# Kernel tuning notes

Measured on AMD Instinct MI355X. Metric: run time of the kernel, lower is better.

Reference implementation:

```python
import jax, jax.numpy as jnp
import numpy as np

N_HEADS, N_LEVELS, N_POINTS = 8, 3, 4


def _bilinear_sample(valf, Hl, Wl, grid):
    """torch.F.grid_sample(mode='bilinear', padding_mode='zeros', align_corners=False).
    valf: [B, nH, hd, Hl*Wl] flattened per-head value map
    grid: [B, Q, nH, P, 2] normalized (x, y) in [-1, 1]
    returns [B, nH, hd, Q, P]
    """
    B, Q, nH, P, _ = grid.shape
    hd = valf.shape[2]
    # unnormalize (align_corners=False)
    ix = ((grid[..., 0] + 1.0) * Wl - 1.0) * 0.5  # [B,Q,nH,P]
    iy = ((grid[..., 1] + 1.0) * Hl - 1.0) * 0.5
    x0 = jnp.floor(ix); y0 = jnp.floor(iy)
    x1 = x0 + 1.0;      y1 = y0 + 1.0
    # corner weights
    w00 = (x1 - ix) * (y1 - iy)
    w01 = (ix - x0) * (y1 - iy)
    w10 = (x1 - ix) * (iy - y0)
    w11 = (ix - x0) * (iy - y0)

    def gather(xi, yi):
        inb = (xi >= 0) & (xi <= Wl - 1) & (yi >= 0) & (yi <= Hl - 1)  # zero padding
        xc = jnp.clip(xi, 0, Wl - 1).astype(jnp.int32)
        yc = jnp.clip(yi, 0, Hl - 1).astype(jnp.int32)
        idx = yc * Wl + xc                              # [B,Q,nH,P]
        idx = idx.transpose(0, 2, 1, 3).reshape(B, nH, 1, Q * P)
        idx = jnp.broadcast_to(idx, (B, nH, hd, Q * P))
        g = jnp.take_along_axis(valf, idx, axis=3)      # [B,nH,hd,Q*P]
        g = g.reshape(B, nH, hd, Q, P)
        mask = inb.transpose(0, 2, 1, 3)[:, :, None, :, :]
        return g * mask

    def w_(w):  # [B,Q,nH,P] -> [B,nH,1,Q,P]
        return w.transpose(0, 2, 1, 3)[:, :, None, :, :]

    return (gather(x0, y0) * w_(w00) + gather(x1, y0) * w_(w01)
            + gather(x0, y1) * w_(w10) + gather(x1, y1) * w_(w11))


def _deform_attn(query, feats, reference_points,
                 W_off, b_off, W_attn, b_attn, W_val, b_val, W_out, b_out):
    B, Q, D = query.shape
    nH, L, P = N_HEADS, N_LEVELS, N_POINTS
    hd = D // nH
    # sampling offsets: tanh * 0.5
    off = jnp.tanh(query @ W_off + b_off).reshape(B, Q, nH, L, P, 2) * 0.5
    # attention weights: softmax over levels*points
    aw = jax.nn.softmax((query @ W_attn + b_attn).reshape(B, Q, nH, L * P), axis=-1)
    aw = aw.reshape(B, Q, nH, L, P)

    out = jnp.zeros((B, Q, nH, hd), dtype=query.dtype)
    for lvl, feat in enumerate(feats):
        Hl, Wl = feat.shape[2], feat.shape[3]
        # value projection on flattened map
        v = feat.reshape(B, D, Hl * Wl).transpose(0, 2, 1) @ W_val + b_val  # [B,S,D]
        valf = v.reshape(B, Hl * Wl, nH, hd).transpose(0, 2, 3, 1)          # [B,nH,hd,S]
        grid = (reference_points[:, :, None, None, :] + off[:, :, :, lvl]) * 2.0 - 1.0  # [B,Q,nH,P,2]
        sampled = _bilinear_sample(valf, Hl, Wl, grid)                      # [B,nH,hd,Q,P]
        w = aw[:, :, :, lvl].transpose(0, 2, 1, 3)[:, :, None, :, :]        # [B,nH,1,Q,P]
        out = out + (sampled * w).sum(-1).transpose(0, 3, 1, 2)             # [B,Q,nH,hd]
    return out.reshape(B, Q, D) @ W_out + b_out


def setup_inputs() -> dict:
    key = jax.random.key(0)
    ks = jax.random.split(key, 13)
    B, Q, D = 4, 8400, 256
    return {
        "query": jax.random.normal(ks[0], (B, Q, D), jnp.float32),
        "feat0": jax.random.normal(ks[1], (B, D, 80, 80), jnp.float32),
        "feat1": jax.random.normal(ks[2], (B, D, 40, 40), jnp.float32),
        "feat2": jax.random.normal(ks[3], (B, D, 20, 20), jnp.float32),
        "reference_points": jax.random.uniform(ks[4], (B, Q, 2), jnp.float32),
        "W_off": jax.random.normal(ks[5], (D, N_HEADS * N_LEVELS * N_POINTS * 2), jnp.float32) * 0.02,
        "b_off": jax.random.normal(ks[6], (N_HEADS * N_LEVELS * N_POINTS * 2,), jnp.float32) * 0.02,
        "W_attn": jax.random.normal(ks[7], (D, N_HEADS * N_LEVELS * N_POINTS), jnp.float32) * 0.02,
        "b_attn": jax.random.normal(ks[8], (N_HEADS * N_LEVELS * N_POINTS,), jnp.float32) * 0.02,
        "W_val": jax.random.normal(ks[9], (D, D), jnp.float32) * (1.0 / np.sqrt(D)),
        "b_val": jnp.zeros((D,), jnp.float32),
        "W_out": jax.random.normal(ks[10], (D, D), jnp.float32) * (1.0 / np.sqrt(D)),
        "b_out": jnp.zeros((D,), jnp.float32),
    }


def reference(query, feat0, feat1, feat2, reference_points,
              W_off, b_off, W_attn, b_attn, W_val, b_val, W_out, b_out):
    return _deform_attn(query, [feat0, feat1, feat2], reference_points,
                        W_off, b_off, W_attn, b_attn, W_val, b_val, W_out, b_out)
```

## Files before the change

### kernel.cpp

```cpp
#include <hip/hip_runtime.h>
#include <math.h>

#define NH    8
#define NPT   4
#define DIM   256
#define NQ    8400
#define BATCH 4
#define STOT  8400
#define MQ    (BATCH * NQ)

typedef __attribute__((ext_vector_type(8))) short  s16x8;
typedef __attribute__((ext_vector_type(8))) unsigned short u16x8;
typedef __attribute__((ext_vector_type(4))) float  f32x4;

static __device__ __forceinline__ unsigned short f2bf(float x) {
    union { float f; unsigned u; } v; v.f = x;
    unsigned r = v.u + 0x7fffu + ((v.u >> 16) & 1u);
    return (unsigned short)(r >> 16);
}
static __device__ __forceinline__ float bf2f(unsigned short h) {
    union { float f; unsigned u; } v; v.u = ((unsigned)h) << 16;
    return v.f;
}

__global__ __launch_bounds__(256) void tp_w(
    const float* __restrict__ W, int Nw,
    unsigned short* __restrict__ outH, unsigned short* __restrict__ outL, int n0)
{
    __shared__ float tile[32][33];
    const int t = threadIdx.x;
    const int nb = blockIdx.x * 32, k0 = blockIdx.y * 32;
    const int c = t & 31, r = t >> 5;
    #pragma unroll
    for (int i = 0; i < 4; ++i) {
        int k = k0 + r + i * 8, n = nb + c;
        tile[r + i * 8][c] = (n < Nw) ? W[(size_t)k * Nw + n] : 0.f;
    }
    __syncthreads();
    #pragma unroll
    for (int i = 0; i < 4; ++i) {
        int n = nb + r + i * 8, k = k0 + c;
        if (n < Nw) {
            float x = tile[c][r + i * 8];
            unsigned short h = f2bf(x);
            outH[(size_t)(n0 + n) * 256 + k] = h;
            if (outL) outL[(size_t)(n0 + n) * 256 + k] = f2bf(x - bf2f(h));
        }
    }
}

__global__ __launch_bounds__(256) void tp_feat(
    const float* __restrict__ feat, int S, int base,
    unsigned short* __restrict__ Abf)
{
    __shared__ float tile[32][33];
    const int t = threadIdx.x;
    const int s0 = blockIdx.x * 32, k0 = blockIdx.y * 32, b = blockIdx.z;
    const int c = t & 31, r = t >> 5;
    #pragma unroll
    for (int i = 0; i < 4; ++i) {
        int k = k0 + r + i * 8, s = s0 + c;
        tile[r + i * 8][c] = (s < S) ? feat[((size_t)b * 256 + k) * S + s] : 0.f;
    }
    __syncthreads();
    #pragma unroll
    for (int i = 0; i < 4; ++i) {
        int s = s0 + r + i * 8, k = k0 + c;
        if (s < S)
            Abf[((size_t)(b * STOT + base + s)) * 256 + k] = f2bf(tile[c][r + i * 8]);
    }
}

__global__ void cat_bias(const float* __restrict__ boff, const float* __restrict__ battn,
                         float* __restrict__ bcat)
{
    int t = blockIdx.x * 256 + threadIdx.x;
    if (t < 192) bcat[t] = boff[t];
    else if (t < 288) bcat[t] = battn[t - 192];
}

template<bool SPLIT, int MODE>
__global__ __launch_bounds__(256) void gemm_bt(
    const void* __restrict__ Aptr,
    const unsigned short* __restrict__ Bh, const unsigned short* __restrict__ Bl,
    const float* __restrict__ bias, void* __restrict__ Cptr,
    int M, int N, int K)
{
    __shared__ unsigned short Ah[128 * 40];
    __shared__ unsigned short Bs[128 * 40];
    __shared__ unsigned short Al[SPLIT ? 128 * 40 : 8];
    __shared__ unsigned short Blo[SPLIT ? 128 * 40 : 8];

    const int t = threadIdx.x;
    const int bn = blockIdx.x * 128, bm = blockIdx.y * 128;
    const int lane = t & 63, w = t >> 6;
    const int wm = (w & 1) * 64, wn = (w >> 1) * 64;
    const int l15 = lane & 15, quad = lane >> 4;

    f32x4 acc[4][4];
    #pragma unroll
    for (int i = 0; i < 4; ++i)
        #pragma unroll
        for (int j = 0; j < 4; ++j)
            acc[i][j] = (f32x4){0.f, 0.f, 0.f, 0.f};

    for (int k0 = 0; k0 < K; k0 += 32) {
        #pragma unroll
        for (int cc = 0; cc < 2; ++cc) {
            int cid = t + cc * 256;
            int r = cid >> 2, s = cid & 3;
            int gr = bm + r; if (gr > M - 1) gr = M - 1;
            if constexpr (SPLIT) {
                const float* ap = (const float*)Aptr + (size_t)gr * K + k0 + s * 8;
                float4 f0 = *(const float4*)ap;
                float4 f1 = *(const float4*)(ap + 4);
                float xs[8] = {f0.x, f0.y, f0.z, f0.w, f1.x, f1.y, f1.z, f1.w};
                u16x8 hv, lv;
                #pragma unroll
                for (int e = 0; e < 8; ++e) {
                    unsigned short h = f2bf(xs[e]);
                    hv[e] = h;
                    lv[e] = f2bf(xs[e] - bf2f(h));
                }
                *(u16x8*)&Ah[r * 40 + s * 8] = hv;
                *(u16x8*)&Al[r * 40 + s * 8] = lv;
            } else {
                u16x8 v = *(const u16x8*)((const unsigned short*)Aptr + (size_t)gr * K + k0 + s * 8);
                *(u16x8*)&Ah[r * 40 + s * 8] = v;
            }
        }
        #pragma unroll
        for (int cc = 0; cc < 2; ++cc) {
            int cid = t + cc * 256;
            int r = cid >> 2, s = cid & 3;
            int gn = bn + r; if (gn > N - 1) gn = N - 1;
            u16x8 v = *(const u16x8*)&Bh[(size_t)gn * K + k0 + s * 8];
            *(u16x8*)&Bs[r * 40 + s * 8] = v;
            if constexpr (SPLIT) {
                u16x8 vl = *(const u16x8*)&Bl[(size_t)gn * K + k0 + s * 8];
                *(u16x8*)&Blo[r * 40 + s * 8] = vl;
            }
        }
        __syncthreads();

        s16x8 af[4], bf[4];
        #pragma unroll
        for (int mt = 0; mt < 4; ++mt)
            af[mt] = *(const s16x8*)&Ah[(wm + mt * 16 + l15) * 40 + quad * 8];
        #pragma unroll
        for (int nt = 0; nt < 4; ++nt)
            bf[nt] = *(const s16x8*)&Bs[(wn + nt * 16 + l15) * 40 + quad * 8];

        if constexpr (SPLIT) {
            s16x8 alf[4], blf[4];
            #pragma unroll
            for (int mt = 0; mt < 4; ++mt)
                alf[mt] = *(const s16x8*)&Al[(wm + mt * 16 + l15) * 40 + quad * 8];
            #pragma unroll
            for (int nt = 0; nt < 4; ++nt)
                blf[nt] = *(const s16x8*)&Blo[(wn + nt * 16 + l15) * 40 + quad * 8];
            #pragma unroll
            for (int mt = 0; mt < 4; ++mt)
                #pragma unroll
                for (int nt = 0; nt < 4; ++nt) {
                    acc[mt][nt] = __builtin_amdgcn_mfma_f32_16x16x32_bf16(af[mt], bf[nt], acc[mt][nt], 0, 0, 0);
                    acc[mt][nt] = __builtin_amdgcn_mfma_f32_16x16x32_bf16(af[mt], blf[nt], acc[mt][nt], 0, 0, 0);
                    acc[mt][nt] = __builtin_amdgcn_mfma_f32_16x16x32_bf16(alf[mt], bf[nt], acc[mt][nt], 0, 0, 0);
                }
        } else {
            #pragma unroll
            for (int mt = 0; mt < 4; ++mt)
                #pragma unroll
                for (int nt = 0; nt < 4; ++nt)
                    acc[mt][nt] = __builtin_amdgcn_mfma_f32_16x16x32_bf16(af[mt], bf[nt], acc[mt][nt], 0, 0, 0);
        }
        __syncthreads();
    }

    #pragma unroll
    for (int nt = 0; nt < 4; ++nt) {
        int col = bn + wn + nt * 16 + l15;
        float bv = (col < N) ? bias[col] : 0.f;
        #pragma unroll
        for (int mt = 0; mt < 4; ++mt) {
            int row0 = bm + wm + mt * 16 + quad * 4;
            #pragma unroll
            for (int r = 0; r < 4; ++r) {
                int row = row0 + r;
                if (row < M && col < N) {
                    float v = acc[mt][nt][r] + bv;
                    if constexpr (MODE == 0) {
                        ((float*)Cptr)[(size_t)row * N + col] = v;
                    } else {
                        int bb = row / STOT, s = row - bb * STOT;
                        int h = col >> 5, c = col & 31;
                        ((unsigned short*)Cptr)[(((size_t)(bb * 8 + h)) * STOT + s) * 32 + c] = f2bf(v);
                    }
                }
            }
        }
    }
}

__global__ __launch_bounds__(256) void sample_v3(
    const unsigned short* __restrict__ valb,
    const float* __restrict__ raw,
    const float* __restrict__ refp,
    unsigned short* __restrict__ out_bf)
{
    const int bq0 = blockIdx.x * 8;
    const int b = bq0 / NQ;
    const int t = threadIdx.x;

    __shared__ int   s_idx[8][96][4];
    __shared__ float s_w[8][96][4];
    __shared__ float s_m[8][8];
    __shared__ float s_inv[8][8];

    if (t < 64) {
        int q = t >> 3, h = t & 7;
        const float* a = &raw[(size_t)(bq0 + q) * 288 + 192 + h * 12];
        float m = a[0];
        #pragma unroll
        for (int j = 1; j < 12; ++j) m = fmaxf(m, a[j]);
        float s = 0.f;
        #pragma unroll
        for (int j = 0; j < 12; ++j) s += expf(a[j] - m);
        s_m[q][h] = m;
        s_inv[q][h] = 1.f / s;
    }
    __syncthreads();

    for (int i = t; i < 768; i += 256) {
        int q = i / 96, p = i - q * 96;
        int h = p / 12, lp = p - h * 12, l = lp >> 2;
        const int dims[3]   = {80, 40, 20};
        const int bases_[3] = {0, 6400, 8000};
        int Wl = dims[l], base = bases_[l];
        size_t ro = (size_t)(bq0 + q) * 288;
        float logit = raw[ro + 192 + p];
        float aw = expf(logit - s_m[q][h]) * s_inv[q][h];
        float rawx = raw[ro + h * 24 + lp * 2 + 0];
        float rawy = raw[ro + h * 24 + lp * 2 + 1];
        float rx = refp[(size_t)(bq0 + q) * 2];
        float ry = refp[(size_t)(bq0 + q) * 2 + 1];
        float ix = (rx + tanhf(rawx) * 0.5f) * Wl - 0.5f;
        float iy = (ry + tanhf(rawy) * 0.5f) * Wl - 0.5f;
        float x0f = floorf(ix), y0f = floorf(iy);
        float fx = ix - x0f, fy = iy - y0f;
        int x0 = (int)x0f, y0 = (int)y0f;
        float w00 = (1.f - fx) * (1.f - fy) * aw;
        float w01 = fx * (1.f - fy) * aw;
        float w10 = (1.f - fx) * fy * aw;
        float w11 = fx * fy * aw;
        bool vx0 = (unsigned)x0 < (unsigned)Wl;
        bool vx1 = (unsigned)(x0 + 1) < (unsigned)Wl;
        bool vy0 = (unsigned)y0 < (unsigned)Wl;
        bool vy1 = (unsigned)(y0 + 1) < (unsigned)Wl;
        int row0 = base + y0 * Wl, row1 = row0 + Wl;
        s_idx[q][p][0] = (vx0 && vy0) ? row0 + x0     : 0;  s_w[q][p][0] = (vx0 && vy0) ? w00 : 0.f;
        s_idx[q][p][1] = (vx1 && vy0) ? row0 + x0 + 1 : 0;  s_w[q][p][1] = (vx1 && vy0) ? w01 : 0.f;
        s_idx[q][p][2] = (vx0 && vy1) ? row1 + x0     : 0;  s_w[q][p][2] = (vx0 && vy1) ? w10 : 0.f;
        s_idx[q][p][3] = (vx1 && vy1) ? row1 + x0 + 1 : 0;  s_w[q][p][3] = (vx1 && vy1) ? w11 : 0.f;
    }
    __syncthreads();

    const int q = t >> 5;
    const int h = (t >> 2) & 7;
    const int l4 = t & 3;
    const unsigned short* vb = valb + ((size_t)(b * 8 + h) * STOT) * 32 + l4 * 8;
    const int*   ip = &s_idx[q][h * 12][0];
    const float* wp = &s_w[q][h * 12][0];
    float acc[8] = {};
    #pragma unroll
    for (int pp = 0; pp < 4; ++pp) {
        int   ix[12]; float ww[12]; u16x8 v[12];
        #pragma unroll
        for (int k = 0; k < 12; ++k) { ix[k] = ip[pp * 12 + k]; ww[k] = wp[pp * 12 + k]; }
        #pragma unroll
        for (int k = 0; k < 12; ++k) v[k] = *(const u16x8*)(vb + (size_t)ix[k] * 32);
        #pragma unroll
        for (int k = 0; k < 12; ++k)
            #pragma unroll
            for (int c = 0; c < 8; ++c)
                acc[c] = fmaf(ww[k], bf2f(v[k][c]), acc[c]);
    }

    u16x8 ob;
    #pragma unroll
    for (int c = 0; c < 8; ++c) ob[c] = f2bf(acc[c]);
    *(u16x8*)&out_bf[(size_t)(bq0 + q) * 256 + h * 32 + l4 * 8] = ob;
}

extern "C" void kernel_launch(void* const* d_in, const int* in_sizes, int n_in,
                              void* d_out, int out_size, void* d_ws, size_t ws_size,
                              hipStream_t stream)
{
    const float* query  = (const float*)d_in[0];
    const float* feat0  = (const float*)d_in[1];
    const float* feat1  = (const float*)d_in[2];
    const float* feat2  = (const float*)d_in[3];
    const float* refp   = (const float*)d_in[4];
    const float* W_off  = (const float*)d_in[5];
    const float* b_off  = (const float*)d_in[6];
    const float* W_attn = (const float*)d_in[7];
    const float* b_attn = (const float*)d_in[8];
    const float* W_val  = (const float*)d_in[9];
    const float* b_val  = (const float*)d_in[10];
    const float* W_out  = (const float*)d_in[11];
    const float* b_out  = (const float*)d_in[12];
    float* out = (float*)d_out;

    unsigned short* valb = (unsigned short*)d_ws;
    float*          raw  = (float*)(valb + (size_t)MQ * 256);
    unsigned short* Abf  = (unsigned short*)(raw + (size_t)MQ * 288);
    unsigned short* outb = Abf;
    unsigned short* Wvt  = Abf + (size_t)MQ * 256;
    unsigned short* Wot  = Wvt + 256 * 256;
    unsigned short* Wch  = Wot + 256 * 256;
    unsigned short* Wcl  = Wch + 288 * 256;
    float*          bcat = (float*)(Wcl + 288 * 256);

    dim3 blk(256);

    tp_w<<<dim3(8, 8), blk, 0, stream>>>(W_val, 256, Wvt, nullptr, 0);
    tp_w<<<dim3(8, 8), blk, 0, stream>>>(W_out, 256, Wot, nullptr, 0);
    tp_w<<<dim3(6, 8), blk, 0, stream>>>(W_off, 192, Wch, Wcl, 0);
    tp_w<<<dim3(3, 8), blk, 0, stream>>>(W_attn, 96, Wch, Wcl, 192);
    cat_bias<<<dim3(2), blk, 0, stream>>>(b_off, b_attn, bcat);
    tp_feat<<<dim3(200, 8, BATCH), blk, 0, stream>>>(feat0, 6400, 0, Abf);
    tp_feat<<<dim3(50, 8, BATCH), blk, 0, stream>>>(feat1, 1600, 6400, Abf);
    tp_feat<<<dim3(13, 8, BATCH), blk, 0, stream>>>(feat2, 400, 8000, Abf);

    gemm_bt<false, 1><<<dim3(2, 263), blk, 0, stream>>>(Abf, Wvt, nullptr, b_val, valb, MQ, 256, 256);
    gemm_bt<true, 0><<<dim3(3, 263), blk, 0, stream>>>(query, Wch, Wcl, bcat, raw, MQ, 288, 256);
    sample_v3<<<dim3(MQ / 8), blk, 0, stream>>>(valb, raw, refp, outb);
    gemm_bt<false, 0><<<dim3(2, 263), blk, 0, stream>>>(outb, Wot, nullptr, b_out, out, MQ, 256, 256);
}
```

Baseline: 281.0 us.

## Merge prep and projection kernels into fewer launches, store attention logits in bf16

Collapses the four weight-transpose launches and the bias concat into one prep kernel. The three feature transposes and the query hi/lo bf16 split now run in one kernel. The value and offset/attention projection GEMMs become a single launch, and the sampler uses an XCD-aware block-to-query mapping and reads attention logits stored as bf16. This cuts launch count and tail effects, at the cost of extra memory traffic for the pre-split query buffers and reduced logit precision.

```diff
diff --git a/kernel.cpp b/kernel.cpp
--- a/kernel.cpp
+++ b/kernel.cpp
@@ -2,7 +2,6 @@
 #include <math.h>
 
 #define NH    8
-#define NPT   4
 #define DIM   256
 #define NQ    8400
 #define BATCH 4
@@ -23,13 +22,32 @@
     return v.f;
 }
 
-__global__ __launch_bounds__(256) void tp_w(
-    const float* __restrict__ W, int Nw,
-    unsigned short* __restrict__ outH, unsigned short* __restrict__ outL, int n0)
-{
+__global__ __launch_bounds__(256) void prep_w(
+    const float* __restrict__ W_val, const float* __restrict__ W_out,
+    const float* __restrict__ W_off, const float* __restrict__ W_attn,
+    const float* __restrict__ b_off, const float* __restrict__ b_attn,
+    unsigned short* __restrict__ Wvt, unsigned short* __restrict__ Wot,
+    unsigned short* __restrict__ Wch, unsigned short* __restrict__ Wcl,
+    float* __restrict__ bcat)
+{
+    const int z = blockIdx.z;
+    const int t = threadIdx.x;
+    if (z == 4) {
+        if (blockIdx.x == 0 && blockIdx.y == 0)
+            for (int i = t; i < 288; i += 256)
+                bcat[i] = (i < 192) ? b_off[i] : b_attn[i - 192];
+        return;
+    }
+    const float* W; unsigned short *oH, *oL; int Nw, n0;
+    switch (z) {
+        case 0:  W = W_val;  oH = Wvt; oL = nullptr; Nw = 256; n0 = 0;   break;
+        case 1:  W = W_out;  oH = Wot; oL = nullptr; Nw = 256; n0 = 0;   break;
+        case 2:  W = W_off;  oH = Wch; oL = Wcl;     Nw = 192; n0 = 0;   break;
+        default: W = W_attn; oH = Wch; oL = Wcl;     Nw = 96;  n0 = 192; break;
+    }
+    const int nb = blockIdx.x * 32, k0 = blockIdx.y * 32;
+    if (nb >= Nw) return;
     __shared__ float tile[32][33];
-    const int t = threadIdx.x;
-    const int nb = blockIdx.x * 32, k0 = blockIdx.y * 32;
     const int c = t & 31, r = t >> 5;
     #pragma unroll
     for (int i = 0; i < 4; ++i) {
@@ -43,54 +61,189 @@
         if (n < Nw) {
             float x = tile[c][r + i * 8];
             unsigned short h = f2bf(x);
-            outH[(size_t)(n0 + n) * 256 + k] = h;
-            if (outL) outL[(size_t)(n0 + n) * 256 + k] = f2bf(x - bf2f(h));
-        }
-    }
-}
-
-__global__ __launch_bounds__(256) void tp_feat(
-    const float* __restrict__ feat, int S, int base,
-    unsigned short* __restrict__ Abf)
-{
+            oH[(size_t)(n0 + n) * 256 + k] = h;
+            if (oL) oL[(size_t)(n0 + n) * 256 + k] = f2bf(x - bf2f(h));
+        }
+    }
+}
+
+__global__ __launch_bounds__(256) void prep_af(
+    const float* __restrict__ feat0, const float* __restrict__ feat1,
+    const float* __restrict__ feat2, const float* __restrict__ query,
+    unsigned short* __restrict__ Abf,
+    unsigned short* __restrict__ Qh, unsigned short* __restrict__ Ql)
+{
+    const int z = blockIdx.z;
+    const int t = threadIdx.x;
+    if (z >= 4) {
+        int lid = (z - 4) * 263 * 8 + blockIdx.x * 8 + blockIdx.y;
+        size_t idx = (size_t)lid * 1024 + t * 4;
+        if (idx < (size_t)MQ * 256) {
+            float4 q = *(const float4*)(query + idx);
+            float xs[4] = {q.x, q.y, q.z, q.w};
+            ushort4 hv, lv;
+            unsigned short h;
+            h = f2bf(xs[0]); hv.x = h; lv.x = f2bf(xs[0] - bf2f(h));
+            h = f2bf(xs[1]); hv.y = h; lv.y = f2bf(xs[1] - bf2f(h));
+            h = f2bf(xs[2]); hv.z = h; lv.z = f2bf(xs[2] - bf2f(h));
+            h = f2bf(xs[3]); hv.w = h; lv.w = f2bf(xs[3] - bf2f(h));
+            *(ushort4*)(Qh + idx) = hv;
+            *(ushort4*)(Ql + idx) = lv;
+        }
+        return;
+    }
+    const int b = z;
+    const int s0 = blockIdx.x * 32, k0 = blockIdx.y * 32;
+    const float* f0b = feat0 + (size_t)b * 256 * 6400;
+    const float* f1b = feat1 + (size_t)b * 256 * 1600;
+    const float* f2b = feat2 + (size_t)b * 256 * 400;
     __shared__ float tile[32][33];
-    const int t = threadIdx.x;
-    const int s0 = blockIdx.x * 32, k0 = blockIdx.y * 32, b = blockIdx.z;
     const int c = t & 31, r = t >> 5;
     #pragma unroll
     for (int i = 0; i < 4; ++i) {
-        int k = k0 + r + i * 8, s = s0 + c;
-        tile[r + i * 8][c] = (s < S) ? feat[((size_t)b * 256 + k) * S + s] : 0.f;
+        int rr = r + i * 8;
+        int s = s0 + c;
+        float v = 0.f;
+        if (s < 8400) {
+            const float* fp; int S, sl;
+            if (s < 6400)      { fp = f0b; S = 6400; sl = s; }
+            else if (s < 8000) { fp = f1b; S = 1600; sl = s - 6400; }
+            else               { fp = f2b; S = 400;  sl = s - 8000; }
+            v = fp[(size_t)(k0 + rr) * S + sl];
+        }
+        tile[rr][c] = v;
     }
     __syncthreads();
     #pragma unroll
     for (int i = 0; i < 4; ++i) {
         int s = s0 + r + i * 8, k = k0 + c;
-        if (s < S)
-            Abf[((size_t)(b * STOT + base + s)) * 256 + k] = f2bf(tile[c][r + i * 8]);
-    }
-}
-
-__global__ void cat_bias(const float* __restrict__ boff, const float* __restrict__ battn,
-                         float* __restrict__ bcat)
-{
-    int t = blockIdx.x * 256 + threadIdx.x;
-    if (t < 192) bcat[t] = boff[t];
-    else if (t < 288) bcat[t] = battn[t - 192];
-}
-
-template<bool SPLIT, int MODE>
-__global__ __launch_bounds__(256) void gemm_bt(
-    const void* __restrict__ Aptr,
-    const unsigned short* __restrict__ Bh, const unsigned short* __restrict__ Bl,
-    const float* __restrict__ bias, void* __restrict__ Cptr,
-    int M, int N, int K)
+        if (s < 8400)
+            Abf[((size_t)b * 8400 + s) * 256 + k] = f2bf(tile[c][r + i * 8]);
+    }
+}
+
+__global__ __launch_bounds__(256) void gemm_vr(
+    const unsigned short* __restrict__ Abf,
+    const unsigned short* __restrict__ Qh, const unsigned short* __restrict__ Ql,
+    const unsigned short* __restrict__ Wvt,
+    const unsigned short* __restrict__ Wch, const unsigned short* __restrict__ Wcl,
+    const float* __restrict__ b_val, const float* __restrict__ bcat,
+    unsigned short* __restrict__ valb, float* __restrict__ raw_off,
+    unsigned short* __restrict__ attnb)
 {
     __shared__ unsigned short Ah[128 * 40];
     __shared__ unsigned short Bs[128 * 40];
-    __shared__ unsigned short Al[SPLIT ? 128 * 40 : 8];
-    __shared__ unsigned short Blo[SPLIT ? 128 * 40 : 8];
-
+    __shared__ unsigned short Al[128 * 40];
+    __shared__ unsigned short Bl2[128 * 40];
+
+    const bool split = blockIdx.x >= 2;
+    const int bn = split ? (blockIdx.x - 2) * 128 : blockIdx.x * 128;
+    const int bm = blockIdx.y * 128;
+    const int N = split ? 288 : 256;
+    const unsigned short* Ag = split ? Qh : Abf;
+    const unsigned short* Bg = split ? Wch : Wvt;
+
+    const int t = threadIdx.x;
+    const int lane = t & 63, w = t >> 6;
+    const int wm = (w & 1) * 64, wn = (w >> 1) * 64;
+    const int l15 = lane & 15, quad = lane >> 4;
+
+    f32x4 acc[4][4];
+    #pragma unroll
+    for (int i = 0; i < 4; ++i)
+        #pragma unroll
+        for (int j = 0; j < 4; ++j)
+            acc[i][j] = (f32x4){0.f, 0.f, 0.f, 0.f};
+
+    for (int k0 = 0; k0 < 256; k0 += 32) {
+        #pragma unroll
+        for (int cc = 0; cc < 2; ++cc) {
+            int cid = t + cc * 256;
+            int r = cid >> 2, s = cid & 3;
+            int gr = bm + r; if (gr > MQ - 1) gr = MQ - 1;
+            u16x8 v = *(const u16x8*)(Ag + (size_t)gr * 256 + k0 + s * 8);
+            *(u16x8*)&Ah[r * 40 + s * 8] = v;
+            if (split) {
+                u16x8 vl = *(const u16x8*)(Ql + (size_t)gr * 256 + k0 + s * 8);
+                *(u16x8*)&Al[r * 40 + s * 8] = vl;
+            }
+            int gn = bn + r; if (gn > N - 1) gn = N - 1;
+            u16x8 bv = *(const u16x8*)(Bg + (size_t)gn * 256 + k0 + s * 8);
+            *(u16x8*)&Bs[r * 40 + s * 8] = bv;
+            if (split) {
+                u16x8 bl = *(const u16x8*)(Wcl + (size_t)gn * 256 + k0 + s * 8);
+                *(u16x8*)&Bl2[r * 40 + s * 8] = bl;
+            }
+        }
+        __syncthreads();
+
+        s16x8 af[4], bfv[4];
+        #pragma unroll
+        for (int mt = 0; mt < 4; ++mt)
+            af[mt] = *(const s16x8*)&Ah[(wm + mt * 16 + l15) * 40 + quad * 8];
+        #pragma unroll
+        for (int nt = 0; nt < 4; ++nt)
+            bfv[nt] = *(const s16x8*)&Bs[(wn + nt * 16 + l15) * 40 + quad * 8];
+
+        if (split) {
+            s16x8 alf[4], blf[4];
+            #pragma unroll
+            for (int mt = 0; mt < 4; ++mt)
+                alf[mt] = *(const s16x8*)&Al[(wm + mt * 16 + l15) * 40 + quad * 8];
+            #pragma unroll
+            for (int nt = 0; nt < 4; ++nt)
+                blf[nt] = *(const s16x8*)&Bl2[(wn + nt * 16 + l15) * 40 + quad * 8];
+            #pragma unroll
+            for (int mt = 0; mt < 4; ++mt)
+                #pragma unroll
+                for (int nt = 0; nt < 4; ++nt) {
+                    acc[mt][nt] = __builtin_amdgcn_mfma_f32_16x16x32_bf16(af[mt], bfv[nt], acc[mt][nt], 0, 0, 0);
+                    acc[mt][nt] = __builtin_amdgcn_mfma_f32_16x16x32_bf16(af[mt], blf[nt], acc[mt][nt], 0, 0, 0);
+                    acc[mt][nt] = __builtin_amdgcn_mfma_f32_16x16x32_bf16(alf[mt], bfv[nt], acc[mt][nt], 0, 0, 0);
+                }
+        } else {
+            #pragma unroll
+            for (int mt = 0; mt < 4; ++mt)
+                #pragma unroll
+                for (int nt = 0; nt < 4; ++nt)
+                    acc[mt][nt] = __builtin_amdgcn_mfma_f32_16x16x32_bf16(af[mt], bfv[nt], acc[mt][nt], 0, 0, 0);
+        }
+        __syncthreads();
+    }
+
+    #pragma unroll
+    for (int nt = 0; nt < 4; ++nt) {
+        int col = bn + wn + nt * 16 + l15;
+        float bv = (col < N) ? (split ? bcat[col] : b_val[col]) : 0.f;
+        #pragma unroll
+        for (int mt = 0; mt < 4; ++mt) {
+            int row0 = bm + wm + mt * 16 + quad * 4;
+            #pragma unroll
+            for (int r = 0; r < 4; ++r) {
+                int row = row0 + r;
+                if (row < MQ && col < N) {
+                    float v = acc[mt][nt][r] + bv;
+                    if (!split) {
+                        int bb = row / STOT, s = row - bb * STOT;
+                        int h = col >> 5, c = col & 31;
+                        valb[(((size_t)(bb * 8 + h)) * STOT + s) * 32 + c] = f2bf(v);
+                    } else if (col < 192) {
+                        raw_off[(size_t)row * 192 + col] = v;
+                    } else {
+                        attnb[(size_t)row * 96 + (col - 192)] = f2bf(v);
+                    }
+                }
+            }
+        }
+    }
+}
+
+__global__ __launch_bounds__(256) void gemm_o(
+    const unsigned short* __restrict__ A, const unsigned short* __restrict__ Bt,
+    const float* __restrict__ bias, float* __restrict__ C)
+{
+    __shared__ unsigned short Ah[128 * 40];
+    __shared__ unsigned short Bs[128 * 40];
     const int t = threadIdx.x;
     const int bn = blockIdx.x * 128, bm = blockIdx.y * 128;
     const int lane = t & 63, w = t >> 6;
@@ -104,112 +257,59 @@
         for (int j = 0; j < 4; ++j)
             acc[i][j] = (f32x4){0.f, 0.f, 0.f, 0.f};
 
-    for (int k0 = 0; k0 < K; k0 += 32) {
+    for (int k0 = 0; k0 < 256; k0 += 32) {
         #pragma unroll
         for (int cc = 0; cc < 2; ++cc) {
             int cid = t + cc * 256;
             int r = cid >> 2, s = cid & 3;
-            int gr = bm + r; if (gr > M - 1) gr = M - 1;
-            if constexpr (SPLIT) {
-                const float* ap = (const float*)Aptr + (size_t)gr * K + k0 + s * 8;
-                float4 f0 = *(const float4*)ap;
-                float4 f1 = *(const float4*)(ap + 4);
-                float xs[8] = {f0.x, f0.y, f0.z, f0.w, f1.x, f1.y, f1.z, f1.w};
-                u16x8 hv, lv;
-                #pragma unroll
-                for (int e = 0; e < 8; ++e) {
-                    unsigned short h = f2bf(xs[e]);
-                    hv[e] = h;
-                    lv[e] = f2bf(xs[e] - bf2f(h));
-                }
-                *(u16x8*)&Ah[r * 40 + s * 8] = hv;
-                *(u16x8*)&Al[r * 40 + s * 8] = lv;
-            } else {
-                u16x8 v = *(const u16x8*)((const unsigned short*)Aptr + (size_t)gr * K + k0 + s * 8);
-                *(u16x8*)&Ah[r * 40 + s * 8] = v;
-            }
-        }
-        #pragma unroll
-        for (int cc = 0; cc < 2; ++cc) {
-            int cid = t + cc * 256;
-            int r = cid >> 2, s = cid & 3;
-            int gn = bn + r; if (gn > N - 1) gn = N - 1;
-            u16x8 v = *(const u16x8*)&Bh[(size_t)gn * K + k0 + s * 8];
-            *(u16x8*)&Bs[r * 40 + s * 8] = v;
-            if constexpr (SPLIT) {
-                u16x8 vl = *(const u16x8*)&Bl[(size_t)gn * K + k0 + s * 8];
-                *(u16x8*)&Blo[r * 40 + s * 8] = vl;
-            }
+            int gr = bm + r; if (gr > MQ - 1) gr = MQ - 1;
+            *(u16x8*)&Ah[r * 40 + s * 8] = *(const u16x8*)(A + (size_t)gr * 256 + k0 + s * 8);
+            *(u16x8*)&Bs[r * 40 + s * 8] = *(const u16x8*)(Bt + (size_t)(bn + r) * 256 + k0 + s * 8);
         }
         __syncthreads();
-
-        s16x8 af[4], bf[4];
+        s16x8 af[4], bfv[4];
         #pragma unroll
         for (int mt = 0; mt < 4; ++mt)
             af[mt] = *(const s16x8*)&Ah[(wm + mt * 16 + l15) * 40 + quad * 8];
         #pragma unroll
         for (int nt = 0; nt < 4; ++nt)
-            bf[nt] = *(const s16x8*)&Bs[(wn + nt * 16 + l15) * 40 + quad * 8];
-
-        if constexpr (SPLIT) {
-            s16x8 alf[4], blf[4];
-            #pragma unroll
-            for (int mt = 0; mt < 4; ++mt)
-                alf[mt] = *(const s16x8*)&Al[(wm + mt * 16 + l15) * 40 + quad * 8];
+            bfv[nt] = *(const s16x8*)&Bs[(wn + nt * 16 + l15) * 40 + quad * 8];
+        #pragma unroll
+        for (int mt = 0; mt < 4; ++mt)
             #pragma unroll
             for (int nt = 0; nt < 4; ++nt)
-                blf[nt] = *(const s16x8*)&Blo[(wn + nt * 16 + l15) * 40 + quad * 8];
-            #pragma unroll
-            for (int mt = 0; mt < 4; ++mt)
-                #pragma unroll
-                for (int nt = 0; nt < 4; ++nt) {
-                    acc[mt][nt] = __builtin_amdgcn_mfma_f32_16x16x32_bf16(af[mt], bf[nt], acc[mt][nt], 0, 0, 0);
-                    acc[mt][nt] = __builtin_amdgcn_mfma_f32_16x16x32_bf16(af[mt], blf[nt], acc[mt][nt], 0, 0, 0);
-                    acc[mt][nt] = __builtin_amdgcn_mfma_f32_16x16x32_bf16(alf[mt], bf[nt], acc[mt][nt], 0, 0, 0);
-                }
-        } else {
-            #pragma unroll
-            for (int mt = 0; mt < 4; ++mt)
-                #pragma unroll
-                for (int nt = 0; nt < 4; ++nt)
-                    acc[mt][nt] = __builtin_amdgcn_mfma_f32_16x16x32_bf16(af[mt], bf[nt], acc[mt][nt], 0, 0, 0);
-        }
+                acc[mt][nt] = __builtin_amdgcn_mfma_f32_16x16x32_bf16(af[mt], bfv[nt], acc[mt][nt], 0, 0, 0);
         __syncthreads();
     }
-
     #pragma unroll
     for (int nt = 0; nt < 4; ++nt) {
         int col = bn + wn + nt * 16 + l15;
-        float bv = (col < N) ? bias[col] : 0.f;
+        float bv = bias[col];
         #pragma unroll
         for (int mt = 0; mt < 4; ++mt) {
             int row0 = bm + wm + mt * 16 + quad * 4;
             #pragma unroll
             for (int r = 0; r < 4; ++r) {
                 int row = row0 + r;
-                if (row < M && col < N) {
-                    float v = acc[mt][nt][r] + bv;
-                    if constexpr (MODE == 0) {
-                        ((float*)Cptr)[(size_t)row * N + col] = v;
-                    } else {
-                        int bb = row / STOT, s = row - bb * STOT;
-                        int h = col >> 5, c = col & 31;
-                        ((unsigned short*)Cptr)[(((size_t)(bb * 8 + h)) * STOT + s) * 32 + c] = f2bf(v);
-                    }
-                }
+                if (row < MQ)
+                    C[(size_t)row * 256 + col] = acc[mt][nt][r] + bv;
             }
         }
     }
 }
 
-__global__ __launch_bounds__(256) void sample_v3(
+__global__ __launch_bounds__(256) void sample_v4(
     const unsigned short* __restrict__ valb,
-    const float* __restrict__ raw,
+    const float* __restrict__ raw_off,
+    const unsigned short* __restrict__ attnb,
     const float* __restrict__ refp,
     unsigned short* __restrict__ out_bf)
 {
-    const int bq0 = blockIdx.x * 8;
-    const int b = bq0 / NQ;
+    const int bx = blockIdx.x;
+    const int xcd = bx & 7;
+    const int b = xcd >> 1;
+    const int qi = (bx >> 3) * 2 + (xcd & 1);
+    const int bq0 = b * NQ + qi * 8;
     const int t = threadIdx.x;
 
     __shared__ int   s_idx[8][96][4];
@@ -219,13 +319,13 @@
 
     if (t < 64) {
         int q = t >> 3, h = t & 7;
-        const float* a = &raw[(size_t)(bq0 + q) * 288 + 192 + h * 12];
-        float m = a[0];
-        #pragma unroll
-        for (int j = 1; j < 12; ++j) m = fmaxf(m, a[j]);
+        const unsigned short* a = attnb + (size_t)(bq0 + q) * 96 + h * 12;
+        float m = bf2f(a[0]);
+        #pragma unroll
+        for (int j = 1; j < 12; ++j) m = fmaxf(m, bf2f(a[j]));
         float s = 0.f;
         #pragma unroll
-        for (int j = 0; j < 12; ++j) s += expf(a[j] - m);
+        for (int j = 0; j < 12; ++j) s += expf(bf2f(a[j]) - m);
         s_m[q][h] = m;
         s_inv[q][h] = 1.f / s;
     }
@@ -237,11 +337,10 @@
         const int dims[3]   = {80, 40, 20};
         const int bases_[3] = {0, 6400, 8000};
         int Wl = dims[l], base = bases_[l];
-        size_t ro = (size_t)(bq0 + q) * 288;
-        float logit = raw[ro + 192 + p];
+        float logit = bf2f(attnb[(size_t)(bq0 + q) * 96 + p]);
         float aw = expf(logit - s_m[q][h]) * s_inv[q][h];
-        float rawx = raw[ro + h * 24 + lp * 2 + 0];
-        float rawy = raw[ro + h * 24 + lp * 2 + 1];
+        size_t ro = (size_t)(bq0 + q) * 192 + h * 24 + lp * 2;
+        float rawx = raw_off[ro], rawy = raw_off[ro + 1];
         float rx = refp[(size_t)(bq0 + q) * 2];
         float ry = refp[(size_t)(bq0 + q) * 2 + 1];
         float ix = (rx + tanhf(rawx) * 0.5f) * Wl - 0.5f;
@@ -285,7 +384,6 @@
             for (int c = 0; c < 8; ++c)
                 acc[c] = fmaf(ww[k], bf2f(v[k][c]), acc[c]);
     }
-
     u16x8 ob;
     #pragma unroll
     for (int c = 0; c < 8; ++c) ob[c] = f2bf(acc[c]);
@@ -311,29 +409,26 @@
     const float* b_out  = (const float*)d_in[12];
     float* out = (float*)d_out;
 
-    unsigned short* valb = (unsigned short*)d_ws;
-    float*          raw  = (float*)(valb + (size_t)MQ * 256);
-    unsigned short* Abf  = (unsigned short*)(raw + (size_t)MQ * 288);
-    unsigned short* outb = Abf;
-    unsigned short* Wvt  = Abf + (size_t)MQ * 256;
-    unsigned short* Wot  = Wvt + 256 * 256;
-    unsigned short* Wch  = Wot + 256 * 256;
-    unsigned short* Wcl  = Wch + 288 * 256;
-    float*          bcat = (float*)(Wcl + 288 * 256);
+    unsigned short* valb  = (unsigned short*)d_ws;
+    float*          rawo  = (float*)(valb + (size_t)MQ * 256);
+    unsigned short* attnb = (unsigned short*)(rawo + (size_t)MQ * 192);
+    unsigned short* Abf   = attnb + (size_t)MQ * 96;
+    unsigned short* outb  = Abf;
+    unsigned short* Qh    = Abf + (size_t)MQ * 256;
+    unsigned short* Ql    = Qh + (size_t)MQ * 256;
+    unsigned short* Wvt   = Ql + (size_t)MQ * 256;
+    unsigned short* Wot   = Wvt + 65536;
+    unsigned short* Wch   = Wot + 65536;
+    unsigned short* Wcl   = Wch + 73728;
+    float*          bcat  = (float*)(Wcl + 73728);
 
     dim3 blk(256);
 
-    tp_w<<<dim3(8, 8), blk, 0, stream>>>(W_val, 256, Wvt, nullptr, 0);
-    tp_w<<<dim3(8, 8), blk, 0, stream>>>(W_out, 256, Wot, nullptr, 0);
-    tp_w<<<dim3(6, 8), blk, 0, stream>>>(W_off, 192, Wch, Wcl, 0);
-    tp_w<<<dim3(3, 8), blk, 0, stream>>>(W_attn, 96, Wch, Wcl, 192);
-    cat_bias<<<dim3(2), blk, 0, stream>>>(b_off, b_attn, bcat);
-    tp_feat<<<dim3(200, 8, BATCH), blk, 0, stream>>>(feat0, 6400, 0, Abf);
-    tp_feat<<<dim3(50, 8, BATCH), blk, 0, stream>>>(feat1, 1600, 6400, Abf);
-    tp_feat<<<dim3(13, 8, BATCH), blk, 0, stream>>>(feat2, 400, 8000, Abf);
-
-    gemm_bt<false, 1><<<dim3(2, 263), blk, 0, stream>>>(Abf, Wvt, nullptr, b_val, valb, MQ, 256, 256);
-    gemm_bt<true, 0><<<dim3(3, 263), blk, 0, stream>>>(query, Wch, Wcl, bcat, raw, MQ, 288, 256);
-    sample_v3<<<dim3(MQ / 8), blk, 0, stream>>>(valb, raw, refp, outb);
-    gemm_bt<false, 0><<<dim3(2, 263), blk, 0, stream>>>(outb, Wot, nullptr, b_out, out, MQ, 256, 256);
-}
+    prep_w<<<dim3(8, 8, 5), blk, 0, stream>>>(W_val, W_out, W_off, W_attn,
+                                              b_off, b_attn, Wvt, Wot, Wch, Wcl, bcat);
+    prep_af<<<dim3(263, 8, 8), blk, 0, stream>>>(feat0, feat1, feat2, query, Abf, Qh, Ql);
+    gemm_vr<<<dim3(5, 263), blk, 0, stream>>>(Abf, Qh, Ql, Wvt, Wch, Wcl,
+                                              b_val, bcat, valb, rawo, attnb);
+    sample_v4<<<dim3(MQ / 8), blk, 0, stream>>>(valb, rawo, attnb, refp, outb);
+    gemm_o<<<dim3(2, 263), blk, 0, stream>>>(outb, Wot, b_out, out);
+}
```

Measured after the change: 286.8 us. +2.1%, slower.
